# Kernel optimization log

Hardware: AMD Instinct MI355X
Metric: run time of the kernel (lower is better)

Reference implementation:

```python
import jax, jax.numpy as jnp
import numpy as np
from jax import lax

T = 6  # max_message_length


def setup_inputs() -> dict:
    key = jax.random.key(0)
    ks = jax.random.split(key, 10)
    B, VIS, H, E, V = 8192, 512, 256, 64, 4096
    s = lambda k, shp, fan: jax.random.normal(k, shp, jnp.float32) * (1.0 / np.sqrt(fan))
    return {
        "vision_feat": jax.random.normal(ks[0], (B, VIS), jnp.float32),
        "Wv": s(ks[1], (VIS, H), VIS),
        "bv": jnp.zeros((H,), jnp.float32),
        "gru_kernel": s(ks[2], (E, 3 * H), E),          # input kernel [z|r|h]
        "gru_rec_kernel": s(ks[3], (H, 3 * H), H),      # recurrent kernel [z|r|h]
        "gru_bias_in": jnp.zeros((3 * H,), jnp.float32),
        "gru_bias_rec": jnp.zeros((3 * H,), jnp.float32),
        "Wo": s(ks[4], (H, V), H),
        "bo": jnp.zeros((V,), jnp.float32),
        "emb": s(ks[5], (V, E), E),
    }


def _gru_cell(x, h, k, rk, b_in, b_rec):
    # Keras GRUCell, reset_after=True
    H = h.shape[1]
    xm = x @ k + b_in          # [B, 3H]
    hm = h @ rk + b_rec        # [B, 3H]
    xz, xr, xh = xm[:, :H], xm[:, H:2 * H], xm[:, 2 * H:]
    hz, hr, hh = hm[:, :H], hm[:, H:2 * H], hm[:, 2 * H:]
    z = jax.nn.sigmoid(xz + hz)
    r = jax.nn.sigmoid(xr + hr)
    hh_t = jnp.tanh(xh + r * hh)
    return z * h + (1.0 - z) * hh_t


def reference(vision_feat, Wv, bv, gru_kernel, gru_rec_kernel, gru_bias_in,
              gru_bias_rec, Wo, bo, emb):
    B = vision_feat.shape[0]
    # NOTE: original code never feeds h_t back as GRU state; state is fixed.
    prev_hidden = vision_feat @ Wv + bv            # [B, H]
    cell0 = jnp.zeros((B, emb.shape[1]), vision_feat.dtype)

    def step(cell_input, _):
        h = _gru_cell(cell_input, prev_hidden, gru_kernel, gru_rec_kernel,
                      gru_bias_in, gru_bias_rec)
        lp = jax.nn.log_softmax(h @ Wo + bo, axis=1)      # [B, V]
        ent = -jnp.sum(lp * jnp.exp(lp), axis=1)          # [B]
        sym = jnp.argmax(lp, axis=1)                      # greedy (training=False)
        sel = jnp.take_along_axis(lp, sym[:, None], axis=1)[:, 0]
        return emb[sym], (sym, sel, ent, h)

    _, (syms, sels, ents, hs) = lax.scan(step, cell0, None, length=T)
    sequence = syms.T.astype(jnp.float32)                 # [B, T]
    logits = sels.T                                       # [B, T]
    entropy = jnp.mean(ents, axis=0)                      # [B]
    message_length = jnp.full((B,), float(T), jnp.float32)
    h_t = hs[-1]                                          # [B, H]
    return sequence, logits, entropy, message_length, h_t
```

## Files before the change

### kernel.cpp

```cpp
#include <hip/hip_runtime.h>
#include <hip/hip_fp16.h>
#include <math.h>


typedef __attribute__((ext_vector_type(8))) _Float16 half8v;
typedef __attribute__((ext_vector_type(4))) float f32x4;

__device__ __forceinline__ int lds_off(int row, int slot) {
    return (row << 6) + ((slot ^ (row & 3) ^ ((row >> 2) & 3)) << 4);
}

__device__ __forceinline__ void gld_lds16(const void* src, void* dst) {
    __builtin_amdgcn_global_load_lds(
        (const __attribute__((address_space(1))) void*)src,
        (__attribute__((address_space(3))) void*)dst, 16, 0, 0);
}

template<int C>
__device__ __forceinline__ float dppf(float x) {
    return __builtin_bit_cast(float, __builtin_amdgcn_update_dpp(
        __builtin_bit_cast(int, x), __builtin_bit_cast(int, x), C, 0xF, 0xF, false));
}
template<int C>
__device__ __forceinline__ int dppi(int x) {
    return __builtin_amdgcn_update_dpp(x, x, C, 0xF, 0xF, false);
}

__device__ __forceinline__ void f16split(float v, unsigned short& u0,
                                         unsigned short& u1) {
    __half a = __float2half(v);
    float f = __half2float(a);
    __half b = __float2half(v - f);
    u0 = __half_as_ushort(a);
    u1 = __half_as_ushort(b);
}

__global__ __launch_bounds__(256) void split_ew(
    const float* __restrict__ in, unsigned short* __restrict__ o0,
    unsigned short* __restrict__ o1, int n4)
{
    int i = blockIdx.x * 256 + threadIdx.x;
    if (i >= n4) return;
    float4 v = *(const float4*)&in[(size_t)i * 4];
    unsigned short a[4], b[4];
    f16split(v.x, a[0], b[0]); f16split(v.y, a[1], b[1]);
    f16split(v.z, a[2], b[2]); f16split(v.w, a[3], b[3]);
    *(uint2*)&o0[(size_t)i * 4] = *(uint2*)a;
    *(uint2*)&o1[(size_t)i * 4] = *(uint2*)b;
}

__global__ __launch_bounds__(256) void trans_split(
    const float* __restrict__ W, unsigned short* __restrict__ o0,
    unsigned short* __restrict__ o1, int N, int K)
{
    __shared__ float Ts[64][65];
    const int tid = threadIdx.x;
    const int n0 = blockIdx.x * 64, k0 = blockIdx.y * 64;
    const int ty = tid >> 2, tx = tid & 3;
    #pragma unroll
    for (int q = 0; q < 4; ++q) {
        float4 v = *(const float4*)&W[(size_t)(k0 + ty) * N + n0 + tx * 16 + q * 4];
        Ts[ty][tx * 16 + q * 4 + 0] = v.x; Ts[ty][tx * 16 + q * 4 + 1] = v.y;
        Ts[ty][tx * 16 + q * 4 + 2] = v.z; Ts[ty][tx * 16 + q * 4 + 3] = v.w;
    }
    __syncthreads();
    #pragma unroll
    for (int ii = 0; ii < 2; ++ii) {
        int item = tid + (ii << 8);
        int n = item >> 3, g = item & 7;
        unsigned short u0[8], u1[8];
        #pragma unroll
        for (int e = 0; e < 8; ++e)
            f16split(Ts[g * 8 + e][n], u0[e], u1[e]);
        size_t base = (size_t)(n0 + n) * K + k0 + g * 8;
        *(uint4*)&o0[base] = *(uint4*)u0;
        *(uint4*)&o1[base] = *(uint4*)u1;
    }
}

template<int KTOT, bool SPLIT>
__global__ __launch_bounds__(256) void mfma_gemm(
    const unsigned short* __restrict__ a0s, const unsigned short* __restrict__ a1s,
    const unsigned short* __restrict__ b0s, const unsigned short* __restrict__ b1s,
    const float* __restrict__ bias, float* __restrict__ C, int ldc,
    unsigned short* __restrict__ s0, unsigned short* __restrict__ s1)
{
    __shared__ char lds[16384];
    const int tid = threadIdx.x;
    const int w = tid >> 6, lane = tid & 63;
    const int c16 = lane & 15, rg = lane >> 4;
    const int m0 = blockIdx.y << 6, n0 = blockIdx.x << 6;
    const int arow0 = (w >> 1) << 5, brow0 = (w & 1) << 5;

    const unsigned short* segsrc = (w == 0) ? a0s : (w == 1) ? a1s
                                 : (w == 2) ? b0s : b1s;
    const int segrow0 = (w < 2) ? m0 : n0;

    f32x4 acc[2][2] = {};

    for (int t = 0; t < KTOT / 32; ++t) {
        const int k0 = t << 5;
        #pragma unroll
        for (int q = 0; q < 4; ++q) {
            int row = (q << 4) + (lane >> 2);
            int slot = (lane & 3) ^ (row & 3) ^ ((row >> 2) & 3);
            gld_lds16(segsrc + (size_t)(segrow0 + row) * KTOT + k0 + (slot << 3),
                      &lds[(w << 12) + (q << 10)]);
        }
        asm volatile("s_waitcnt vmcnt(0)" ::: "memory");
        __syncthreads();
        half8v afr[2][2], bfr[2][2];
        #pragma unroll
        for (int i = 0; i < 2; ++i) {
            int oa = lds_off(arow0 + (i << 4) + c16, rg);
            afr[i][0] = *(half8v*)&lds[oa];
            afr[i][1] = *(half8v*)&lds[4096 + oa];
            int ob = lds_off(brow0 + (i << 4) + c16, rg);
            bfr[i][0] = *(half8v*)&lds[8192 + ob];
            bfr[i][1] = *(half8v*)&lds[12288 + ob];
        }
        #pragma unroll
        for (int i = 0; i < 2; ++i)
            #pragma unroll
            for (int j = 0; j < 2; ++j) {
                f32x4 c = acc[i][j];
                c = __builtin_amdgcn_mfma_f32_16x16x32_f16(afr[i][0], bfr[j][0], c, 0, 0, 0);
                c = __builtin_amdgcn_mfma_f32_16x16x32_f16(afr[i][1], bfr[j][0], c, 0, 0, 0);
                c = __builtin_amdgcn_mfma_f32_16x16x32_f16(afr[i][0], bfr[j][1], c, 0, 0, 0);
                acc[i][j] = c;
            }
        __syncthreads();
    }

    #pragma unroll
    for (int j = 0; j < 2; ++j) {
        int col = n0 + brow0 + (j << 4) + c16;
        float bb = bias[col];
        #pragma unroll
        for (int i = 0; i < 2; ++i)
            #pragma unroll
            for (int reg = 0; reg < 4; ++reg) {
                int row = m0 + arow0 + (i << 4) + (rg << 2) + reg;
                float v = acc[i][j][reg] + bb;
                C[(size_t)row * ldc + col] = v;
                if (SPLIT) {
                    unsigned short u0, u1;
                    f16split(v, u0, u1);
                    s0[(size_t)row * ldc + col] = u0;
                    s1[(size_t)row * ldc + col] = u1;
                }
            }
    }
}

__global__ __launch_bounds__(256) void gru_fused(
    const float4* __restrict__ pstats, const float* __restrict__ emb,
    const float* __restrict__ gk, const float* __restrict__ b_in,
    const float* __restrict__ hm, const float* __restrict__ ph,
    unsigned short* __restrict__ h0, unsigned short* __restrict__ h1,
    float* __restrict__ ht_out, float* __restrict__ out_seq,
    float* __restrict__ out_sel, float* __restrict__ out_ent, int t)
{
    __shared__ float xsT[64][8];
    __shared__ int syms_lds[8];
    const int tid = threadIdx.x;
    const int row0 = blockIdx.x * 8;
    float az[8], ar[8], ah[8];
    const float bz = b_in[tid], br = b_in[256 + tid], bh = b_in[512 + tid];
    #pragma unroll
    for (int r = 0; r < 8; ++r) { az[r] = bz; ar[r] = br; ah[r] = bh; }

    if (t > 0) {
        const int r = tid >> 5, p = tid & 31;
        const int row = row0 + r;
        float4 pa = pstats[(size_t)p * 8192 + row];
        float4 pb = pstats[(size_t)(p + 32) * 8192 + row];
        float M = pa.x, S = pa.y + pb.y, Q = pa.z + pb.z;
        int A = __float_as_int(pa.w);
        { int a2 = __float_as_int(pb.w);
          if (pb.x > M || (pb.x == M && a2 < A)) { M = pb.x; A = a2; } }
        #pragma unroll
        for (int off = 1; off < 32; off <<= 1) {
            float m2 = __shfl_xor(M, off);
            float s2 = __shfl_xor(S, off);
            float q2 = __shfl_xor(Q, off);
            int   a2 = __shfl_xor(A, off);
            S += s2; Q += q2;
            if (m2 > M || (m2 == M && a2 < A)) { M = m2; A = a2; }
        }
        if (p == 0) {
            float lse = logf(S);
            float sel = M - lse;
            float ent = lse - Q / S;
            out_seq[(size_t)row * 6 + (t - 1)] = (float)A;
            out_sel[(size_t)row * 6 + (t - 1)] = sel;
            float ea = (t == 1) ? ent : (out_ent[row] + ent);
            out_ent[row] = ea;
            syms_lds[r] = A;
        }
        __syncthreads();
        for (int l = tid; l < 512; l += 256) {
            int r2 = l >> 6, e = l & 63;
            xsT[e][r2] = emb[(size_t)syms_lds[r2] * 64 + e];
        }
        __syncthreads();
        #pragma unroll 4
        for (int e = 0; e < 64; ++e) {
            float kz  = gk[e * 768 + tid];
            float kr_ = gk[e * 768 + 256 + tid];
            float kh  = gk[e * 768 + 512 + tid];
            float4 x0 = *(float4*)&xsT[e][0];
            float4 x1 = *(float4*)&xsT[e][4];
            float xv[8] = {x0.x, x0.y, x0.z, x0.w, x1.x, x1.y, x1.z, x1.w};
            #pragma unroll
            for (int r2 = 0; r2 < 8; ++r2) {
                az[r2] = fmaf(xv[r2], kz, az[r2]);
                ar[r2] = fmaf(xv[r2], kr_, ar[r2]);
                ah[r2] = fmaf(xv[r2], kh, ah[r2]);
            }
        }
    }
    #pragma unroll
    for (int r = 0; r < 8; ++r) {
        const int row = row0 + r;
        float hz  = hm[(size_t)row * 768 + tid];
        float hr  = hm[(size_t)row * 768 + 256 + tid];
        float hh  = hm[(size_t)row * 768 + 512 + tid];
        float phv = ph[(size_t)row * 256 + tid];
        float z  = 1.0f / (1.0f + __expf(-(az[r] + hz)));
        float rr = 1.0f / (1.0f + __expf(-(ar[r] + hr)));
        float ht = tanhf(ah[r] + rr * hh);
        float hv = z * phv + (1.0f - z) * ht;
        size_t idx = (size_t)row * 256 + tid;
        unsigned short u0, u1;
        f16split(hv, u0, u1);
        h0[idx] = u0; h1[idx] = u1;
        if (ht_out) ht_out[idx] = hv;
    }
}

__global__ __launch_bounds__(256, 3) void logits_mfma(
    const unsigned short* __restrict__ h0, const unsigned short* __restrict__ h1,
    const unsigned short* __restrict__ w0, const unsigned short* __restrict__ w1,
    const float* __restrict__ bo, float4* __restrict__ pstats)
{
    __shared__ char lds[32768];
    const int tid = threadIdx.x;
    const int w = tid >> 6, lane = tid & 63;
    const int c16 = lane & 15, rg = lane >> 4;
    const int m0 = blockIdx.y << 7, n0 = blockIdx.x << 7;
    const int arow0 = (w >> 1) << 6, brow0 = (w & 1) << 6;

    const unsigned short* segsrc = (w == 0) ? h0 : (w == 1) ? h1
                                 : (w == 2) ? w0 : w1;
    const int segrow0 = (w < 2) ? m0 : n0;

    f32x4 acc[4][4] = {};

    for (int t = 0; t < 8; ++t) {
        const int k0 = t << 5;
        #pragma unroll
        for (int q = 0; q < 8; ++q) {
            int row = (q << 4) + (lane >> 2);
            int slot = (lane & 3) ^ (row & 3) ^ ((row >> 2) & 3);
            gld_lds16(segsrc + (size_t)(segrow0 + row) * 256 + k0 + (slot << 3),
                      &lds[(w << 13) + (q << 10)]);
        }
        asm volatile("s_waitcnt vmcnt(0)" ::: "memory");
        __syncthreads();
        half8v afr[4][2];
        #pragma unroll
        for (int i = 0; i < 4; ++i) {
            int o = lds_off(arow0 + (i << 4) + c16, rg);
            afr[i][0] = *(half8v*)&lds[o];
            afr[i][1] = *(half8v*)&lds[8192 + o];
        }
        #pragma unroll
        for (int j = 0; j < 4; ++j) {
            int o = lds_off(brow0 + (j << 4) + c16, rg);
            half8v b0 = *(half8v*)&lds[16384 + o];
            half8v b1 = *(half8v*)&lds[24576 + o];
            #pragma unroll
            for (int i = 0; i < 4; ++i) {
                f32x4 c = acc[i][j];
                c = __builtin_amdgcn_mfma_f32_16x16x32_f16(afr[i][0], b0, c, 0, 0, 0);
                c = __builtin_amdgcn_mfma_f32_16x16x32_f16(afr[i][1], b0, c, 0, 0, 0);
                c = __builtin_amdgcn_mfma_f32_16x16x32_f16(afr[i][0], b1, c, 0, 0, 0);
                acc[i][j] = c;
            }
        }
        __syncthreads();
    }

    const int wn0 = n0 + brow0;
    float bov[4];
    #pragma unroll
    for (int j = 0; j < 4; ++j) bov[j] = bo[wn0 + j * 16 + c16];
    #pragma unroll
    for (int i = 0; i < 4; ++i) {
        #pragma unroll
        for (int reg = 0; reg < 4; ++reg) {
            float l0 = acc[i][0][reg] + bov[0];
            float l1 = acc[i][1][reg] + bov[1];
            float l2 = acc[i][2][reg] + bov[2];
            float l3 = acc[i][3][reg] + bov[3];
            float m = l0; int a = wn0 + c16;
            if (l1 > m) { m = l1; a = wn0 + 16 + c16; }
            if (l2 > m) { m = l2; a = wn0 + 32 + c16; }
            if (l3 > m) { m = l3; a = wn0 + 48 + c16; }
            float e0 = __expf(l0), e1 = __expf(l1), e2 = __expf(l2), e3 = __expf(l3);
            float s = (e0 + e1) + (e2 + e3);
            float q = fmaf(l0, e0, fmaf(l1, e1, fmaf(l2, e2, l3 * e3)));
            s += dppf<0x108>(s); s += dppf<0x104>(s);
            s += dppf<0x102>(s); s += dppf<0x101>(s);
            q += dppf<0x108>(q); q += dppf<0x104>(q);
            q += dppf<0x102>(q); q += dppf<0x101>(q);
            #define MMERGE(C) { float m2 = dppf<C>(m); int a2 = dppi<C>(a); \
                bool bt = (m2 > m) || (m2 == m && a2 < a); \
                m = bt ? m2 : m; a = bt ? a2 : a; }
            MMERGE(0x108) MMERGE(0x104) MMERGE(0x102) MMERGE(0x101)
            #undef MMERGE
            if (c16 == 0) {
                int grow = m0 + arow0 + (i << 4) + (rg << 2) + reg;
                pstats[(size_t)((blockIdx.x << 1) + (w & 1)) * 8192 + grow] =
                    make_float4(m, s, q, __int_as_float(a));
            }
        }
    }
}

__global__ __launch_bounds__(64) void finalize_kernel(
    const float4* __restrict__ pstats, float* __restrict__ out_seq,
    float* __restrict__ out_sel, float* __restrict__ out_ent,
    float* __restrict__ out_ml)
{
    const int row = blockIdx.x * 64 + threadIdx.x;
    float M = -INFINITY, S = 0.f, Q = 0.f; int A = 0;
    #pragma unroll 8
    for (int p = 0; p < 64; ++p) {
        float4 pp = pstats[(size_t)p * 8192 + row];
        S += pp.y; Q += pp.z;
        int a2 = __float_as_int(pp.w);
        if (pp.x > M || (pp.x == M && a2 < A)) { M = pp.x; A = a2; }
    }
    float lse = logf(S);
    float sel = M - lse;
    float ent = lse - Q / S;
    out_seq[(size_t)row * 6 + 5] = (float)A;
    out_sel[(size_t)row * 6 + 5] = sel;
    out_ent[row] = (out_ent[row] + ent) * (1.0f / 6.0f);
    out_ml[row] = 6.0f;
}

extern "C" void kernel_launch(void* const* d_in, const int* in_sizes, int n_in,
                              void* d_out, int out_size, void* d_ws, size_t ws_size,
                              hipStream_t stream) {
    const float* vis  = (const float*)d_in[0];
    const float* Wv   = (const float*)d_in[1];
    const float* bv   = (const float*)d_in[2];
    const float* gk   = (const float*)d_in[3];
    const float* grk  = (const float*)d_in[4];
    const float* bin  = (const float*)d_in[5];
    const float* brec = (const float*)d_in[6];
    const float* Wo   = (const float*)d_in[7];
    const float* bo   = (const float*)d_in[8];
    const float* emb  = (const float*)d_in[9];

    float* out = (float*)d_out;
    float* out_seq = out;
    float* out_sel = out + 49152;
    float* out_ent = out + 98304;
    float* out_ml  = out + 106496;
    float* out_ht  = out + 114688;

    char* ws = (char*)d_ws;
    float*          ph     = (float*)(ws);
    float*          hm     = (float*)(ws + 8388608);
    unsigned short* vis0   = (unsigned short*)(ws + 8388608);
    unsigned short* vis1   = (unsigned short*)(ws + 16777216);
    unsigned short* h0     = (unsigned short*)(ws + 33554432);
    unsigned short* h1     = (unsigned short*)(ws + 37748736);
    unsigned short* w0     = (unsigned short*)(ws + 41943040);
    unsigned short* w1     = (unsigned short*)(ws + 44040192);
    float4*         pstats = (float4*)(ws + 46137344);
    unsigned short* ph0    = (unsigned short*)(ws + 46137344);
    unsigned short* ph1    = (unsigned short*)(ws + 50331648);
    unsigned short* wv0    = (unsigned short*)(ws + 54558720);
    unsigned short* wv1    = (unsigned short*)(ws + 54820864);
    unsigned short* g0     = (unsigned short*)(ws + 55083008);
    unsigned short* g1     = (unsigned short*)(ws + 55476224);

    trans_split<<<dim3(64, 4), 256, 0, stream>>>(Wo, w0, w1, 4096, 256);
    trans_split<<<dim3(4, 8), 256, 0, stream>>>(Wv, wv0, wv1, 256, 512);
    trans_split<<<dim3(12, 4), 256, 0, stream>>>(grk, g0, g1, 768, 256);
    split_ew<<<4096, 256, 0, stream>>>(vis, vis0, vis1, 1048576);

    mfma_gemm<512, true><<<dim3(4, 128), 256, 0, stream>>>(
        vis0, vis1, wv0, wv1, bv, ph, 256, ph0, ph1);
    mfma_gemm<256, false><<<dim3(12, 128), 256, 0, stream>>>(
        ph0, ph1, g0, g1, brec, hm, 768, nullptr, nullptr);

    for (int t = 0; t < 6; ++t) {
        gru_fused<<<1024, 256, 0, stream>>>(pstats, emb, gk, bin, hm, ph,
                                            h0, h1,
                                            (t == 5) ? out_ht : nullptr,
                                            out_seq, out_sel, out_ent, t);
        logits_mfma<<<dim3(32, 64), 256, 0, stream>>>(h0, h1, w0, w1, bo, pstats);
    }
    finalize_kernel<<<128, 64, 0, stream>>>(pstats, out_seq, out_sel,
                                            out_ent, out_ml);
}
```

Before: 559.8 us.

## Load MFMA operands directly from global into registers with double buffering

The logits GEMM kernel drops its LDS staging (global_load_lds plus barriers). Each wave now loads its A and B fragments straight from global memory into registers, using two register sets so the next K-slice loads while the current one feeds the MFMAs. Occupancy is lowered to 2 blocks per SM to fit the extra registers. It also swaps tanhf and logf for cheaper exp-based and intrinsic versions. The cost is that neighbouring waves no longer share staged tiles, so more global/L2 traffic, and the cheap math is slightly less accurate.

```diff
diff --git a/kernel.cpp b/kernel.cpp
--- a/kernel.cpp
+++ b/kernel.cpp
@@ -33,6 +33,12 @@
     __half b = __float2half(v - f);
     u0 = __half_as_ushort(a);
     u1 = __half_as_ushort(b);
+}
+
+__device__ __forceinline__ float fast_tanh(float x) {
+    float t = __expf(-2.0f * fabsf(x));
+    float th = (1.0f - t) / (1.0f + t);
+    return copysignf(th, x);
 }
 
 __global__ __launch_bounds__(256) void split_ew(
@@ -189,7 +195,7 @@
             if (m2 > M || (m2 == M && a2 < A)) { M = m2; A = a2; }
         }
         if (p == 0) {
-            float lse = logf(S);
+            float lse = __logf(S);
             float sel = M - lse;
             float ent = lse - Q / S;
             out_seq[(size_t)row * 6 + (t - 1)] = (float)A;
@@ -229,7 +235,7 @@
         float phv = ph[(size_t)row * 256 + tid];
         float z  = 1.0f / (1.0f + __expf(-(az[r] + hz)));
         float rr = 1.0f / (1.0f + __expf(-(ar[r] + hr)));
-        float ht = tanhf(ah[r] + rr * hh);
+        float ht = fast_tanh(ah[r] + rr * hh);
         float hv = z * phv + (1.0f - z) * ht;
         size_t idx = (size_t)row * 256 + tid;
         unsigned short u0, u1;
@@ -239,57 +245,77 @@
     }
 }
 
-__global__ __launch_bounds__(256, 3) void logits_mfma(
+__global__ __launch_bounds__(256, 2) void logits_mfma(
     const unsigned short* __restrict__ h0, const unsigned short* __restrict__ h1,
     const unsigned short* __restrict__ w0, const unsigned short* __restrict__ w1,
     const float* __restrict__ bo, float4* __restrict__ pstats)
 {
-    __shared__ char lds[32768];
     const int tid = threadIdx.x;
     const int w = tid >> 6, lane = tid & 63;
     const int c16 = lane & 15, rg = lane >> 4;
     const int m0 = blockIdx.y << 7, n0 = blockIdx.x << 7;
     const int arow0 = (w >> 1) << 6, brow0 = (w & 1) << 6;
 
-    const unsigned short* segsrc = (w == 0) ? h0 : (w == 1) ? h1
-                                 : (w == 2) ? w0 : w1;
-    const int segrow0 = (w < 2) ? m0 : n0;
+    unsigned aoff[4], boff[4];
+    #pragma unroll
+    for (int i = 0; i < 4; ++i) {
+        aoff[i] = (unsigned)(m0 + arow0 + i * 16 + c16) * 256u + rg * 8u;
+        boff[i] = (unsigned)(n0 + brow0 + i * 16 + c16) * 256u + rg * 8u;
+    }
 
     f32x4 acc[4][4] = {};
 
-    for (int t = 0; t < 8; ++t) {
-        const int k0 = t << 5;
-        #pragma unroll
-        for (int q = 0; q < 8; ++q) {
-            int row = (q << 4) + (lane >> 2);
-            int slot = (lane & 3) ^ (row & 3) ^ ((row >> 2) & 3);
-            gld_lds16(segsrc + (size_t)(segrow0 + row) * 256 + k0 + (slot << 3),
-                      &lds[(w << 13) + (q << 10)]);
-        }
-        asm volatile("s_waitcnt vmcnt(0)" ::: "memory");
-        __syncthreads();
-        half8v afr[4][2];
-        #pragma unroll
-        for (int i = 0; i < 4; ++i) {
-            int o = lds_off(arow0 + (i << 4) + c16, rg);
-            afr[i][0] = *(half8v*)&lds[o];
-            afr[i][1] = *(half8v*)&lds[8192 + o];
-        }
-        #pragma unroll
-        for (int j = 0; j < 4; ++j) {
-            int o = lds_off(brow0 + (j << 4) + c16, rg);
-            half8v b0 = *(half8v*)&lds[16384 + o];
-            half8v b1 = *(half8v*)&lds[24576 + o];
+    half8v A0a[4], A1a[4], B0a[4], B1a[4];
+    half8v A0b[4], A1b[4], B0b[4], B1b[4];
+
+    #pragma unroll
+    for (int i = 0; i < 4; ++i) {
+        A0a[i] = *(const half8v*)(h0 + aoff[i]);
+        A1a[i] = *(const half8v*)(h1 + aoff[i]);
+        B0a[i] = *(const half8v*)(w0 + boff[i]);
+        B1a[i] = *(const half8v*)(w1 + boff[i]);
+    }
+
+    #pragma unroll
+    for (int t = 0; t < 8; t += 2) {
+        if (t + 1 < 8) {
+            #pragma unroll
+            for (int i = 0; i < 4; ++i) {
+                A0b[i] = *(const half8v*)(h0 + aoff[i] + (t + 1) * 32);
+                A1b[i] = *(const half8v*)(h1 + aoff[i] + (t + 1) * 32);
+                B0b[i] = *(const half8v*)(w0 + boff[i] + (t + 1) * 32);
+                B1b[i] = *(const half8v*)(w1 + boff[i] + (t + 1) * 32);
+            }
+        }
+        #pragma unroll
+        for (int j = 0; j < 4; ++j)
             #pragma unroll
             for (int i = 0; i < 4; ++i) {
                 f32x4 c = acc[i][j];
-                c = __builtin_amdgcn_mfma_f32_16x16x32_f16(afr[i][0], b0, c, 0, 0, 0);
-                c = __builtin_amdgcn_mfma_f32_16x16x32_f16(afr[i][1], b0, c, 0, 0, 0);
-                c = __builtin_amdgcn_mfma_f32_16x16x32_f16(afr[i][0], b1, c, 0, 0, 0);
+                c = __builtin_amdgcn_mfma_f32_16x16x32_f16(A0a[i], B0a[j], c, 0, 0, 0);
+                c = __builtin_amdgcn_mfma_f32_16x16x32_f16(A1a[i], B0a[j], c, 0, 0, 0);
+                c = __builtin_amdgcn_mfma_f32_16x16x32_f16(A0a[i], B1a[j], c, 0, 0, 0);
                 acc[i][j] = c;
             }
-        }
-        __syncthreads();
+        if (t + 2 < 8) {
+            #pragma unroll
+            for (int i = 0; i < 4; ++i) {
+                A0a[i] = *(const half8v*)(h0 + aoff[i] + (t + 2) * 32);
+                A1a[i] = *(const half8v*)(h1 + aoff[i] + (t + 2) * 32);
+                B0a[i] = *(const half8v*)(w0 + boff[i] + (t + 2) * 32);
+                B1a[i] = *(const half8v*)(w1 + boff[i] + (t + 2) * 32);
+            }
+        }
+        #pragma unroll
+        for (int j = 0; j < 4; ++j)
+            #pragma unroll
+            for (int i = 0; i < 4; ++i) {
+                f32x4 c = acc[i][j];
+                c = __builtin_amdgcn_mfma_f32_16x16x32_f16(A0b[i], B0b[j], c, 0, 0, 0);
+                c = __builtin_amdgcn_mfma_f32_16x16x32_f16(A1b[i], B0b[j], c, 0, 0, 0);
+                c = __builtin_amdgcn_mfma_f32_16x16x32_f16(A0b[i], B1b[j], c, 0, 0, 0);
+                acc[i][j] = c;
+            }
     }
 
     const int wn0 = n0 + brow0;
@@ -343,7 +369,7 @@
         int a2 = __float_as_int(pp.w);
         if (pp.x > M || (pp.x == M && a2 < A)) { M = pp.x; A = a2; }
     }
-    float lse = logf(S);
+    float lse = __logf(S);
     float sel = M - lse;
     float ent = lse - Q / S;
     out_seq[(size_t)row * 6 + 5] = (float)A;
```

New measurement: 936.9 us. +67.4%, slower.

## Double-buffer LDS in logits MFMA kernel and use fast tanh/log intrinsics

Applied to the files above, without the earlier changes.

Rewrites the logits MFMA main loop to double-buffer the LDS tiles, prefetching K-tile t+2 while computing on tile t. Fragments are loaded into registers before the barrier and MFMAs run at raised wave priority. This is meant to hide global-to-LDS load latency that the old loop exposed with a full vmcnt(0) wait every iteration. In exchange it doubles LDS to 64KB and lowers the occupancy hint from 3 to 2 blocks per CU. Separately, tanhf and logf are replaced with exp-based fast_tanh and __logf, which cost a little accuracy.

```diff
diff --git a/kernel.cpp b/kernel.cpp
--- a/kernel.cpp
+++ b/kernel.cpp
@@ -33,6 +33,12 @@
     __half b = __float2half(v - f);
     u0 = __half_as_ushort(a);
     u1 = __half_as_ushort(b);
+}
+
+__device__ __forceinline__ float fast_tanh(float x) {
+    float t = __expf(-2.0f * fabsf(x));
+    float th = (1.0f - t) / (1.0f + t);
+    return copysignf(th, x);
 }
 
 __global__ __launch_bounds__(256) void split_ew(
@@ -189,7 +195,7 @@
             if (m2 > M || (m2 == M && a2 < A)) { M = m2; A = a2; }
         }
         if (p == 0) {
-            float lse = logf(S);
+            float lse = __logf(S);
             float sel = M - lse;
             float ent = lse - Q / S;
             out_seq[(size_t)row * 6 + (t - 1)] = (float)A;
@@ -229,7 +235,7 @@
         float phv = ph[(size_t)row * 256 + tid];
         float z  = 1.0f / (1.0f + __expf(-(az[r] + hz)));
         float rr = 1.0f / (1.0f + __expf(-(ar[r] + hr)));
-        float ht = tanhf(ah[r] + rr * hh);
+        float ht = fast_tanh(ah[r] + rr * hh);
         float hv = z * phv + (1.0f - z) * ht;
         size_t idx = (size_t)row * 256 + tid;
         unsigned short u0, u1;
@@ -239,12 +245,12 @@
     }
 }
 
-__global__ __launch_bounds__(256, 3) void logits_mfma(
+__global__ __launch_bounds__(256, 2) void logits_mfma(
     const unsigned short* __restrict__ h0, const unsigned short* __restrict__ h1,
     const unsigned short* __restrict__ w0, const unsigned short* __restrict__ w1,
     const float* __restrict__ bo, float4* __restrict__ pstats)
 {
-    __shared__ char lds[32768];
+    __shared__ char lds[65536];
     const int tid = threadIdx.x;
     const int w = tid >> 6, lane = tid & 63;
     const int c16 = lane & 15, rg = lane >> 4;
@@ -255,42 +261,72 @@
                                  : (w == 2) ? w0 : w1;
     const int segrow0 = (w < 2) ? m0 : n0;
 
+    #define STAGE(t_, buf_)                                                    \
+    {                                                                          \
+        const int k0_ = (t_) << 5;                                             \
+        _Pragma("unroll")                                                      \
+        for (int q = 0; q < 8; ++q) {                                          \
+            int row_ = (q << 4) + (lane >> 2);                                 \
+            int slot_ = (lane & 3) ^ (row_ & 3) ^ ((row_ >> 2) & 3);           \
+            gld_lds16(segsrc + (size_t)(segrow0 + row_) * 256 + k0_ +          \
+                          (slot_ << 3),                                        \
+                      &lds[((buf_) << 15) + (w << 13) + (q << 10)]);           \
+        }                                                                      \
+    }
+
     f32x4 acc[4][4] = {};
 
+    STAGE(0, 0)
+    STAGE(1, 1)
+    asm volatile("s_waitcnt vmcnt(8)" ::: "memory");
+    __builtin_amdgcn_sched_barrier(0);
+    __builtin_amdgcn_s_barrier();
+
+    #pragma unroll
     for (int t = 0; t < 8; ++t) {
-        const int k0 = t << 5;
-        #pragma unroll
-        for (int q = 0; q < 8; ++q) {
-            int row = (q << 4) + (lane >> 2);
-            int slot = (lane & 3) ^ (row & 3) ^ ((row >> 2) & 3);
-            gld_lds16(segsrc + (size_t)(segrow0 + row) * 256 + k0 + (slot << 3),
-                      &lds[(w << 13) + (q << 10)]);
-        }
-        asm volatile("s_waitcnt vmcnt(0)" ::: "memory");
-        __syncthreads();
-        half8v afr[4][2];
+        const int base = (t & 1) << 15;
+        half8v afr[4][2], bfr[4][2];
         #pragma unroll
         for (int i = 0; i < 4; ++i) {
             int o = lds_off(arow0 + (i << 4) + c16, rg);
-            afr[i][0] = *(half8v*)&lds[o];
-            afr[i][1] = *(half8v*)&lds[8192 + o];
+            afr[i][0] = *(half8v*)&lds[base + o];
+            afr[i][1] = *(half8v*)&lds[base + 8192 + o];
         }
         #pragma unroll
         for (int j = 0; j < 4; ++j) {
             int o = lds_off(brow0 + (j << 4) + c16, rg);
-            half8v b0 = *(half8v*)&lds[16384 + o];
-            half8v b1 = *(half8v*)&lds[24576 + o];
+            bfr[j][0] = *(half8v*)&lds[base + 16384 + o];
+            bfr[j][1] = *(half8v*)&lds[base + 24576 + o];
+        }
+        asm volatile("s_waitcnt lgkmcnt(0)" ::: "memory");
+        __builtin_amdgcn_sched_barrier(0);
+        __builtin_amdgcn_s_barrier();
+        if (t + 2 < 8) STAGE(t + 2, t & 1)
+
+        __builtin_amdgcn_s_setprio(1);
+        #pragma unroll
+        for (int j = 0; j < 4; ++j)
             #pragma unroll
             for (int i = 0; i < 4; ++i) {
                 f32x4 c = acc[i][j];
-                c = __builtin_amdgcn_mfma_f32_16x16x32_f16(afr[i][0], b0, c, 0, 0, 0);
-                c = __builtin_amdgcn_mfma_f32_16x16x32_f16(afr[i][1], b0, c, 0, 0, 0);
-                c = __builtin_amdgcn_mfma_f32_16x16x32_f16(afr[i][0], b1, c, 0, 0, 0);
+                c = __builtin_amdgcn_mfma_f32_16x16x32_f16(afr[i][0], bfr[j][0], c, 0, 0, 0);
+                c = __builtin_amdgcn_mfma_f32_16x16x32_f16(afr[i][1], bfr[j][0], c, 0, 0, 0);
+                c = __builtin_amdgcn_mfma_f32_16x16x32_f16(afr[i][0], bfr[j][1], c, 0, 0, 0);
                 acc[i][j] = c;
             }
-        }
-        __syncthreads();
-    }
+        __builtin_amdgcn_s_setprio(0);
+
+        if (t + 1 < 8) {
+            if (t + 2 < 8) {
+                asm volatile("s_waitcnt vmcnt(8)" ::: "memory");
+            } else {
+                asm volatile("s_waitcnt vmcnt(0)" ::: "memory");
+            }
+            __builtin_amdgcn_sched_barrier(0);
+            __builtin_amdgcn_s_barrier();
+        }
+    }
+    #undef STAGE
 
     const int wn0 = n0 + brow0;
     float bov[4];
@@ -343,7 +379,7 @@
         int a2 = __float_as_int(pp.w);
         if (pp.x > M || (pp.x == M && a2 < A)) { M = pp.x; A = a2; }
     }
-    float lse = logf(S);
+    float lse = __logf(S);
     float sel = M - lse;
     float ent = lse - Q / S;
     out_seq[(size_t)row * 6 + 5] = (float)A;
```

New measurement: 578.6 us. +3.4%, slower.

## Keep Wo panel in registers and stream h strips through double-buffered LDS

Applied to the files above, without the earlier changes.

The logits GEMM now gives each block a 128-column panel of Wo held in registers for the whole K=256. A 512-row strip of h is streamed through double-buffered LDS in 32-row chunks. Partial softmax stats are reduced across the four waves in LDS, which halves the number of pstats partitions (64 to 32), and the gru and finalize reductions are updated to match. The GRU also gets a cheaper exp-based tanh and __logf. The cost is higher register pressure (occupancy hint drops to 2), a 66KB LDS footprint, and a slight loss of accuracy from the approximate tanh and log.

```diff
diff --git a/kernel.cpp b/kernel.cpp
--- a/kernel.cpp
+++ b/kernel.cpp
@@ -33,6 +33,12 @@
     __half b = __float2half(v - f);
     u0 = __half_as_ushort(a);
     u1 = __half_as_ushort(b);
+}
+
+__device__ __forceinline__ float fast_tanh(float x) {
+    float t = __expf(-2.0f * fabsf(x));
+    float th = (1.0f - t) / (1.0f + t);
+    return copysignf(th, x);
 }
 
 __global__ __launch_bounds__(256) void split_ew(
@@ -174,11 +180,8 @@
         const int r = tid >> 5, p = tid & 31;
         const int row = row0 + r;
         float4 pa = pstats[(size_t)p * 8192 + row];
-        float4 pb = pstats[(size_t)(p + 32) * 8192 + row];
-        float M = pa.x, S = pa.y + pb.y, Q = pa.z + pb.z;
+        float M = pa.x, S = pa.y, Q = pa.z;
         int A = __float_as_int(pa.w);
-        { int a2 = __float_as_int(pb.w);
-          if (pb.x > M || (pb.x == M && a2 < A)) { M = pb.x; A = a2; } }
         #pragma unroll
         for (int off = 1; off < 32; off <<= 1) {
             float m2 = __shfl_xor(M, off);
@@ -189,7 +192,7 @@
             if (m2 > M || (m2 == M && a2 < A)) { M = m2; A = a2; }
         }
         if (p == 0) {
-            float lse = logf(S);
+            float lse = __logf(S);
             float sel = M - lse;
             float ent = lse - Q / S;
             out_seq[(size_t)row * 6 + (t - 1)] = (float)A;
@@ -229,7 +232,7 @@
         float phv = ph[(size_t)row * 256 + tid];
         float z  = 1.0f / (1.0f + __expf(-(az[r] + hz)));
         float rr = 1.0f / (1.0f + __expf(-(ar[r] + hr)));
-        float ht = tanhf(ah[r] + rr * hh);
+        float ht = fast_tanh(ah[r] + rr * hh);
         float hv = z * phv + (1.0f - z) * ht;
         size_t idx = (size_t)row * 256 + tid;
         unsigned short u0, u1;
@@ -239,94 +242,129 @@
     }
 }
 
-__global__ __launch_bounds__(256, 3) void logits_mfma(
+__global__ __launch_bounds__(256, 2) void logits_mfma(
     const unsigned short* __restrict__ h0, const unsigned short* __restrict__ h1,
     const unsigned short* __restrict__ w0, const unsigned short* __restrict__ w1,
     const float* __restrict__ bo, float4* __restrict__ pstats)
 {
-    __shared__ char lds[32768];
+    __shared__ char lds[67584];
     const int tid = threadIdx.x;
     const int w = tid >> 6, lane = tid & 63;
     const int c16 = lane & 15, rg = lane >> 4;
-    const int m0 = blockIdx.y << 7, n0 = blockIdx.x << 7;
-    const int arow0 = (w >> 1) << 6, brow0 = (w & 1) << 6;
-
-    const unsigned short* segsrc = (w == 0) ? h0 : (w == 1) ? h1
-                                 : (w == 2) ? w0 : w1;
-    const int segrow0 = (w < 2) ? m0 : n0;
-
-    f32x4 acc[4][4] = {};
-
-    for (int t = 0; t < 8; ++t) {
-        const int k0 = t << 5;
-        #pragma unroll
-        for (int q = 0; q < 8; ++q) {
-            int row = (q << 4) + (lane >> 2);
-            int slot = (lane & 3) ^ (row & 3) ^ ((row >> 2) & 3);
-            gld_lds16(segsrc + (size_t)(segrow0 + row) * 256 + k0 + (slot << 3),
-                      &lds[(w << 13) + (q << 10)]);
+    const int strip_row0 = blockIdx.x << 9;
+    const int npanel = blockIdx.y;
+    const int cols0 = (npanel << 7) + (w << 5);
+
+    half8v B0[8][2], B1[8][2];
+    {
+        size_t b0 = (size_t)(cols0 + c16) * 256 + rg * 8;
+        size_t b1 = (size_t)(cols0 + 16 + c16) * 256 + rg * 8;
+        #pragma unroll
+        for (int t = 0; t < 8; ++t) {
+            B0[t][0] = *(const half8v*)(w0 + b0 + t * 32);
+            B0[t][1] = *(const half8v*)(w0 + b1 + t * 32);
+            B1[t][0] = *(const half8v*)(w1 + b0 + t * 32);
+            B1[t][1] = *(const half8v*)(w1 + b1 + t * 32);
+        }
+    }
+    const float bv0 = bo[cols0 + c16];
+    const float bv1 = bo[cols0 + 16 + c16];
+
+    const unsigned short* hs = (w < 2) ? h0 : h1;
+    const int tb = (w & 1) << 2;
+    const int sseg = (w >> 1) << 14;
+
+    #define STAGE(c_, buf_) {                                                  \
+        const int r0_ = strip_row0 + ((c_) << 5);                              \
+        _Pragma("unroll")                                                      \
+        for (int u = 0; u < 8; ++u) {                                          \
+            const int tt = tb + (u >> 1), ii = u & 1;                          \
+            gld_lds16(hs + (size_t)(r0_ + ii * 16 + c16) * 256 + tt * 32 + rg * 8, \
+                      &lds[((buf_) << 15) + sseg + ((tt * 2 + ii) << 10)]);    \
+        } }
+
+    STAGE(0, 0)
+    asm volatile("s_waitcnt vmcnt(0)" ::: "memory");
+    __syncthreads();
+
+    const int lb = lane << 4;
+    for (int c = 0; c < 16; ++c) {
+        if (c < 15) STAGE(c + 1, (c + 1) & 1)
+        const int base = (c & 1) << 15;
+
+        f32x4 acc[2][2] = {};
+        #pragma unroll
+        for (int t = 0; t < 8; ++t) {
+            half8v a00 = *(half8v*)&lds[base + ((t * 2 + 0) << 10) + lb];
+            half8v a01 = *(half8v*)&lds[base + ((t * 2 + 1) << 10) + lb];
+            half8v a10 = *(half8v*)&lds[base + 16384 + ((t * 2 + 0) << 10) + lb];
+            half8v a11 = *(half8v*)&lds[base + 16384 + ((t * 2 + 1) << 10) + lb];
+            f32x4 c00 = acc[0][0], c01 = acc[0][1], c10 = acc[1][0], c11 = acc[1][1];
+            c00 = __builtin_amdgcn_mfma_f32_16x16x32_f16(a00, B0[t][0], c00, 0, 0, 0);
+            c01 = __builtin_amdgcn_mfma_f32_16x16x32_f16(a00, B0[t][1], c01, 0, 0, 0);
+            c10 = __builtin_amdgcn_mfma_f32_16x16x32_f16(a01, B0[t][0], c10, 0, 0, 0);
+            c11 = __builtin_amdgcn_mfma_f32_16x16x32_f16(a01, B0[t][1], c11, 0, 0, 0);
+            c00 = __builtin_amdgcn_mfma_f32_16x16x32_f16(a10, B0[t][0], c00, 0, 0, 0);
+            c01 = __builtin_amdgcn_mfma_f32_16x16x32_f16(a10, B0[t][1], c01, 0, 0, 0);
+            c10 = __builtin_amdgcn_mfma_f32_16x16x32_f16(a11, B0[t][0], c10, 0, 0, 0);
+            c11 = __builtin_amdgcn_mfma_f32_16x16x32_f16(a11, B0[t][1], c11, 0, 0, 0);
+            c00 = __builtin_amdgcn_mfma_f32_16x16x32_f16(a00, B1[t][0], c00, 0, 0, 0);
+            c01 = __builtin_amdgcn_mfma_f32_16x16x32_f16(a00, B1[t][1], c01, 0, 0, 0);
+            c10 = __builtin_amdgcn_mfma_f32_16x16x32_f16(a01, B1[t][0], c10, 0, 0, 0);
+            c11 = __builtin_amdgcn_mfma_f32_16x16x32_f16(a01, B1[t][1], c11, 0, 0, 0);
+            acc[0][0] = c00; acc[0][1] = c01; acc[1][0] = c10; acc[1][1] = c11;
+        }
+
+        #pragma unroll
+        for (int i = 0; i < 2; ++i) {
+            #pragma unroll
+            for (int reg = 0; reg < 4; ++reg) {
+                float l0 = acc[i][0][reg] + bv0;
+                float l1 = acc[i][1][reg] + bv1;
+                float m; int a;
+                if (l1 > l0) { m = l1; a = cols0 + 16 + c16; }
+                else         { m = l0; a = cols0 + c16; }
+                float e0 = __expf(l0), e1 = __expf(l1);
+                float s = e0 + e1;
+                float q = fmaf(l0, e0, l1 * e1);
+                s += dppf<0x108>(s); s += dppf<0x104>(s);
+                s += dppf<0x102>(s); s += dppf<0x101>(s);
+                q += dppf<0x108>(q); q += dppf<0x104>(q);
+                q += dppf<0x102>(q); q += dppf<0x101>(q);
+                #define MMERGE(C) { float m2 = dppf<C>(m); int a2 = dppi<C>(a); \
+                    bool bt = (m2 > m) || (m2 == m && a2 < a); \
+                    m = bt ? m2 : m; a = bt ? a2 : a; }
+                MMERGE(0x108) MMERGE(0x104) MMERGE(0x102) MMERGE(0x101)
+                #undef MMERGE
+                if (c16 == 0) {
+                    int r_in = i * 16 + (rg << 2) + reg;
+                    *(float4*)&lds[65536 + (((w << 5) + r_in) << 4)] =
+                        make_float4(m, s, q, __int_as_float(a));
+                }
+            }
+        }
+        __syncthreads();
+        if (tid < 32) {
+            float4 p0 = *(float4*)&lds[65536 + (tid << 4)];
+            float4 p1 = *(float4*)&lds[65536 + ((32 + tid) << 4)];
+            float4 p2 = *(float4*)&lds[65536 + ((64 + tid) << 4)];
+            float4 p3 = *(float4*)&lds[65536 + ((96 + tid) << 4)];
+            float M = p0.x, S = p0.y, Q = p0.z; int A = __float_as_int(p0.w);
+            S += p1.y + p2.y + p3.y;
+            Q += p1.z + p2.z + p3.z;
+            { int a2 = __float_as_int(p1.w);
+              if (p1.x > M || (p1.x == M && a2 < A)) { M = p1.x; A = a2; } }
+            { int a2 = __float_as_int(p2.w);
+              if (p2.x > M || (p2.x == M && a2 < A)) { M = p2.x; A = a2; } }
+            { int a2 = __float_as_int(p3.w);
+              if (p3.x > M || (p3.x == M && a2 < A)) { M = p3.x; A = a2; } }
+            pstats[(size_t)npanel * 8192 + strip_row0 + (c << 5) + tid] =
+                make_float4(M, S, Q, __int_as_float(A));
         }
         asm volatile("s_waitcnt vmcnt(0)" ::: "memory");
         __syncthreads();
-        half8v afr[4][2];
-        #pragma unroll
-        for (int i = 0; i < 4; ++i) {
-            int o = lds_off(arow0 + (i << 4) + c16, rg);
-            afr[i][0] = *(half8v*)&lds[o];
-            afr[i][1] = *(half8v*)&lds[8192 + o];
-        }
-        #pragma unroll
-        for (int j = 0; j < 4; ++j) {
-            int o = lds_off(brow0 + (j << 4) + c16, rg);
-            half8v b0 = *(half8v*)&lds[16384 + o];
-            half8v b1 = *(half8v*)&lds[24576 + o];
-            #pragma unroll
-            for (int i = 0; i < 4; ++i) {
-                f32x4 c = acc[i][j];
-                c = __builtin_amdgcn_mfma_f32_16x16x32_f16(afr[i][0], b0, c, 0, 0, 0);
-                c = __builtin_amdgcn_mfma_f32_16x16x32_f16(afr[i][1], b0, c, 0, 0, 0);
-                c = __builtin_amdgcn_mfma_f32_16x16x32_f16(afr[i][0], b1, c, 0, 0, 0);
-                acc[i][j] = c;
-            }
-        }
-        __syncthreads();
-    }
-
-    const int wn0 = n0 + brow0;
-    float bov[4];
-    #pragma unroll
-    for (int j = 0; j < 4; ++j) bov[j] = bo[wn0 + j * 16 + c16];
-    #pragma unroll
-    for (int i = 0; i < 4; ++i) {
-        #pragma unroll
-        for (int reg = 0; reg < 4; ++reg) {
-            float l0 = acc[i][0][reg] + bov[0];
-            float l1 = acc[i][1][reg] + bov[1];
-            float l2 = acc[i][2][reg] + bov[2];
-            float l3 = acc[i][3][reg] + bov[3];
-            float m = l0; int a = wn0 + c16;
-            if (l1 > m) { m = l1; a = wn0 + 16 + c16; }
-            if (l2 > m) { m = l2; a = wn0 + 32 + c16; }
-            if (l3 > m) { m = l3; a = wn0 + 48 + c16; }
-            float e0 = __expf(l0), e1 = __expf(l1), e2 = __expf(l2), e3 = __expf(l3);
-            float s = (e0 + e1) + (e2 + e3);
-            float q = fmaf(l0, e0, fmaf(l1, e1, fmaf(l2, e2, l3 * e3)));
-            s += dppf<0x108>(s); s += dppf<0x104>(s);
-            s += dppf<0x102>(s); s += dppf<0x101>(s);
-            q += dppf<0x108>(q); q += dppf<0x104>(q);
-            q += dppf<0x102>(q); q += dppf<0x101>(q);
-            #define MMERGE(C) { float m2 = dppf<C>(m); int a2 = dppi<C>(a); \
-                bool bt = (m2 > m) || (m2 == m && a2 < a); \
-                m = bt ? m2 : m; a = bt ? a2 : a; }
-            MMERGE(0x108) MMERGE(0x104) MMERGE(0x102) MMERGE(0x101)
-            #undef MMERGE
-            if (c16 == 0) {
-                int grow = m0 + arow0 + (i << 4) + (rg << 2) + reg;
-                pstats[(size_t)((blockIdx.x << 1) + (w & 1)) * 8192 + grow] =
-                    make_float4(m, s, q, __int_as_float(a));
-            }
-        }
-    }
+    }
+    #undef STAGE
 }
 
 __global__ __launch_bounds__(64) void finalize_kernel(
@@ -337,13 +375,13 @@
     const int row = blockIdx.x * 64 + threadIdx.x;
     float M = -INFINITY, S = 0.f, Q = 0.f; int A = 0;
     #pragma unroll 8
-    for (int p = 0; p < 64; ++p) {
+    for (int p = 0; p < 32; ++p) {
         float4 pp = pstats[(size_t)p * 8192 + row];
         S += pp.y; Q += pp.z;
         int a2 = __float_as_int(pp.w);
         if (pp.x > M || (pp.x == M && a2 < A)) { M = pp.x; A = a2; }
     }
-    float lse = logf(S);
+    float lse = __logf(S);
     float sel = M - lse;
     float ent = lse - Q / S;
     out_seq[(size_t)row * 6 + 5] = (float)A;
@@ -405,7 +443,7 @@
                                             h0, h1,
                                             (t == 5) ? out_ht : nullptr,
                                             out_seq, out_sel, out_ent, t);
-        logits_mfma<<<dim3(32, 64), 256, 0, stream>>>(h0, h1, w0, w1, bo, pstats);
+        logits_mfma<<<dim3(16, 32), 256, 0, stream>>>(h0, h1, w0, w1, bo, pstats);
     }
     finalize_kernel<<<128, 64, 0, stream>>>(pstats, out_seq, out_sel,
                                             out_ent, out_ml);
```

Result: slower. 659.5 us (+17.8%).
